# Kernel optimization log

Hardware: AMD Instinct MI355X
Metric: run time of the kernel (lower is better)

Reference implementation:

```python
import jax, jax.numpy as jnp
import numpy as np

N, IN_FEAT, OUT_FEAT = 8192, 512, 256
SLOPE = 0.1


def setup_inputs() -> dict:
    key = jax.random.key(0)
    k1, k2, k3, k4, k5 = jax.random.split(key, 5)
    doc = jax.random.normal(k1, (N, IN_FEAT), dtype=jnp.float32)
    W = jax.random.normal(k2, (IN_FEAT, OUT_FEAT), dtype=jnp.float32) * (1.0 / np.sqrt(IN_FEAT))
    W_b = jax.random.normal(k3, (OUT_FEAT,), dtype=jnp.float32) * 0.01
    a = jax.random.normal(k4, (2 * OUT_FEAT,), dtype=jnp.float32) * (1.0 / np.sqrt(2 * OUT_FEAT))
    a_b = jax.random.normal(k5, (1,), dtype=jnp.float32) * 0.01
    return {"doc": doc, "W": W, "W_b": W_b, "a": a, "a_b": a_b}


def reference(doc, W, W_b, a, a_b):
    # h = W(doc): [N, outFeat]
    h = doc @ W + W_b
    d = h.shape[-1]
    # aParams(cat(h_i, h_j)) = a1.h_i + a2.h_j + b  (avoids the O(N^2*2d) concat)
    a1, a2 = a[:d], a[d:]
    score = (h @ a1)[:, None] + (h @ a2)[None, :] + a_b[0]  # [N, N]
    score = jax.nn.leaky_relu(score, SLOPE)
    # adj=None path -> all-ones mask, the where() is a no-op
    att = jax.nn.softmax(score, axis=1)  # normalize over neighbors j
    out = jax.nn.leaky_relu(att @ h, SLOPE)  # [N, outFeat]
    return out, att
```

## Files before the change

### kernel.cpp

```cpp
#include <hip/hip_runtime.h>
#include <hip/hip_bf16.h>


typedef __attribute__((ext_vector_type(4))) float f32x4;
typedef __attribute__((ext_vector_type(8))) short short8;
typedef __attribute__((ext_vector_type(4))) unsigned short ushort4v;

#define SLOPE 0.1f
#define NROW 8192
#define DDIM 256

__device__ __forceinline__ float lrelu(float x){ return fmaxf(x, SLOPE * x); }

__device__ __forceinline__ unsigned short f2bf(float f){
  union { float f; unsigned u; } v; v.f = f;
  unsigned r = (v.u + 0x7fffu + ((v.u >> 16) & 1u)) >> 16;
  return (unsigned short)r;
}
__device__ __forceinline__ float bf2f(unsigned short u){
  union { unsigned u; float f; } v; v.u = (unsigned)u << 16; return v.f;
}
__device__ __forceinline__ unsigned cvt_pk_bf16(float lo, float hi){
  unsigned r;
  asm("v_cvt_pk_bf16_f32 %0, %1, %2" : "=v"(r) : "v"(lo), "v"(hi));
  return r;
}

__global__ __launch_bounds__(256) void k_prep(
    const float* __restrict__ W,
    unsigned short* __restrict__ Wt_hi, unsigned short* __restrict__ Wt_lo)
{
  const int tid = blockIdx.x * 256 + threadIdx.x;
  const int c = tid >> 7, kq = tid & 127;
  ushort4v hi, lo;
#pragma unroll
  for (int j = 0; j < 4; ++j) {
    const float v = W[(size_t)(kq * 4 + j) * 256 + c];
    hi[j] = f2bf(v);
    lo[j] = f2bf(v - bf2f(hi[j]));
  }
  *reinterpret_cast<ushort4v*>(Wt_hi + (size_t)c * 512 + kq * 4) = hi;
  *reinterpret_cast<ushort4v*>(Wt_lo + (size_t)c * 512 + kq * 4) = lo;
}

__global__ __launch_bounds__(512, 2) void k_h(
    const float* __restrict__ doc, const unsigned short* __restrict__ Wt_hi,
    const unsigned short* __restrict__ Wt_lo, const float* __restrict__ Wb,
    const float* __restrict__ a,
    unsigned short* __restrict__ ht, float* __restrict__ s1,
    float* __restrict__ e2, float* __restrict__ e02)
{
  __shared__ __align__(16) short8 aH[2][2][64];
  __shared__ __align__(16) short8 aL[2][2][64];
  __shared__ float sred[8][2][32];

  const int t = threadIdx.x, w = t >> 6, l = t & 63;
  const int lr = l & 15, lg = l >> 4;
  const int rb = blockIdx.x * 32;
  const int cb = w * 32;

  f32x4 acc[2][2];
#pragma unroll
  for (int rt = 0; rt < 2; ++rt)
#pragma unroll
    for (int ct = 0; ct < 2; ++ct) acc[rt][ct] = (f32x4){0.f, 0.f, 0.f, 0.f};

  const float* docp = doc + (size_t)(rb + w * 16 + lr) * 512 + lg * 8;

  f32x4 v0, v1;
  auto loadDoc = [&](int k0) { if (w < 2) {
      v0 = *reinterpret_cast<const f32x4*>(docp + k0);
      v1 = *reinterpret_cast<const f32x4*>(docp + k0 + 4);
  }};
  auto writeStage = [&](int pb) { if (w < 2) {
      union { short8 v; unsigned short u[8]; } hi, lo;
#pragma unroll
      for (int q = 0; q < 4; ++q) {
        hi.u[q] = f2bf(v0[q]);     lo.u[q] = f2bf(v0[q] - bf2f(hi.u[q]));
        hi.u[4+q] = f2bf(v1[q]);   lo.u[4+q] = f2bf(v1[q] - bf2f(hi.u[4+q]));
      }
      aH[pb][w][l] = hi.v;
      aL[pb][w][l] = lo.v;
  }};

  loadDoc(0); writeStage(0); loadDoc(32);

  for (int n = 0; n < 16; ++n) {
    const int kk = n * 32;
    const int par = n & 1;

    asm volatile("s_waitcnt lgkmcnt(0)\n\ts_barrier" ::: "memory");

    const short8 ah0 = aH[par][0][l];
    const short8 ah1 = aH[par][1][l];
    const short8 al0 = aL[par][0][l];
    const short8 al1 = aL[par][1][l];

    short8 bh[2], bl[2];
#pragma unroll
    for (int ct = 0; ct < 2; ++ct) {
      const size_t off = (size_t)(cb + ct * 16 + lr) * 512 + kk + lg * 8;
      bh[ct] = *reinterpret_cast<const short8*>(Wt_hi + off);
      bl[ct] = *reinterpret_cast<const short8*>(Wt_lo + off);
    }

    if (n + 1 < 16) writeStage(par ^ 1);
    if (n + 2 < 16) loadDoc((n + 2) * 32);

#pragma unroll
    for (int ct = 0; ct < 2; ++ct) {
      acc[0][ct] = __builtin_amdgcn_mfma_f32_16x16x32_bf16(ah0, bh[ct], acc[0][ct], 0, 0, 0);
      acc[1][ct] = __builtin_amdgcn_mfma_f32_16x16x32_bf16(ah1, bh[ct], acc[1][ct], 0, 0, 0);
      acc[0][ct] = __builtin_amdgcn_mfma_f32_16x16x32_bf16(ah0, bl[ct], acc[0][ct], 0, 0, 0);
      acc[1][ct] = __builtin_amdgcn_mfma_f32_16x16x32_bf16(ah1, bl[ct], acc[1][ct], 0, 0, 0);
      acc[0][ct] = __builtin_amdgcn_mfma_f32_16x16x32_bf16(al0, bh[ct], acc[0][ct], 0, 0, 0);
      acc[1][ct] = __builtin_amdgcn_mfma_f32_16x16x32_bf16(al1, bh[ct], acc[1][ct], 0, 0, 0);
    }
  }

  float bias[2];
#pragma unroll
  for (int ct = 0; ct < 2; ++ct) bias[ct] = Wb[cb + ct * 16 + lr];
#pragma unroll
  for (int rt = 0; rt < 2; ++rt)
#pragma unroll
    for (int ct = 0; ct < 2; ++ct) {
#pragma unroll
      for (int q = 0; q < 4; ++q) acc[rt][ct][q] += bias[ct];
      ushort4v u;
#pragma unroll
      for (int q = 0; q < 4; ++q) u[q] = f2bf(acc[rt][ct][q]);
      *reinterpret_cast<ushort4v*>(
          ht + (size_t)(cb + ct * 16 + lr) * 8192 + rb + rt * 16 + lg * 4) = u;
    }

  float a1c[2], a2c[2];
#pragma unroll
  for (int ct = 0; ct < 2; ++ct) {
    a1c[ct] = a[cb + ct * 16 + lr];
    a2c[ct] = a[256 + cb + ct * 16 + lr];
  }
  float p1[2][4], p2[2][4];
#pragma unroll
  for (int rt = 0; rt < 2; ++rt)
#pragma unroll
    for (int q = 0; q < 4; ++q) {
      float x1 = 0.f, x2 = 0.f;
#pragma unroll
      for (int ct = 0; ct < 2; ++ct) {
        x1 = fmaf(acc[rt][ct][q], a1c[ct], x1);
        x2 = fmaf(acc[rt][ct][q], a2c[ct], x2);
      }
#pragma unroll
      for (int off = 1; off < 16; off <<= 1) {
        x1 += __shfl_xor(x1, off);
        x2 += __shfl_xor(x2, off);
      }
      p1[rt][q] = x1; p2[rt][q] = x2;
    }
  __syncthreads();
  if (lr == 0) {
#pragma unroll
    for (int rt = 0; rt < 2; ++rt)
#pragma unroll
      for (int q = 0; q < 4; ++q) {
        sred[w][0][rt * 16 + lg * 4 + q] = p1[rt][q];
        sred[w][1][rt * 16 + lg * 4 + q] = p2[rt][q];
      }
  }
  __syncthreads();
  if (t < 32) {
    float v1s = 0.f, v2s = 0.f;
#pragma unroll
    for (int ww = 0; ww < 8; ++ww) { v1s += sred[ww][0][t]; v2s += sred[ww][1][t]; }
    const int r = rb + t;
    s1[r] = v1s;
    e2[r] = __expf(v2s);
    e02[r] = __expf(SLOPE * v2s);
  }
}

__global__ __launch_bounds__(256) void k_z(
    const float* __restrict__ s1, const float* __restrict__ e2g,
    const float* __restrict__ e02g, const float* __restrict__ abp,
    float* __restrict__ rowinfo)
{
  __shared__ __align__(16) float es[8192];
  __shared__ __align__(16) float fs[8192];
  const int t = threadIdx.x;
  for (int i = t * 4; i < 8192; i += 1024) {
    *reinterpret_cast<f32x4*>(&es[i]) = *reinterpret_cast<const f32x4*>(e2g + i);
    *reinterpret_cast<f32x4*>(&fs[i]) = *reinterpret_cast<const f32x4*>(e02g + i);
  }
  __syncthreads();
  const int w = t >> 6, l = t & 63;
  const float ab = abp[0];
  const int rb = blockIdx.x * 16 + w * 4;
  float T[4], E1[4], E01[4];
#pragma unroll
  for (int rr = 0; rr < 4; ++rr) {
    const float s1a = s1[rb + rr] + ab;
    E1[rr] = __expf(s1a); E01[rr] = __expf(SLOPE * s1a); T[rr] = __expf(-s1a);
  }
  float zA[4] = {0.f,0.f,0.f,0.f}, zB[4] = {0.f,0.f,0.f,0.f};
  for (int i = l * 4; i < 8192; i += 256) {
    const f32x4 e = *reinterpret_cast<const f32x4*>(&es[i]);
    const f32x4 f = *reinterpret_cast<const f32x4*>(&fs[i]);
#pragma unroll
    for (int rr = 0; rr < 4; ++rr)
#pragma unroll
      for (int q = 0; q < 4; ++q) {
        const bool c = (e[q] >= T[rr]);
        zA[rr] += c ? e[q] : 0.f;
        zB[rr] += c ? 0.f : f[q];
      }
  }
#pragma unroll
  for (int rr = 0; rr < 4; ++rr) {
    float z = E1[rr] * zA[rr] + E01[rr] * zB[rr];
#pragma unroll
    for (int off = 32; off > 0; off >>= 1) z += __shfl_down(z, off);
    if (l == 0) {
      const float iz = 1.0f / z;
      f32x4 ri = (f32x4){E1[rr] * iz, E01[rr] * iz, T[rr], iz};
      *reinterpret_cast<f32x4*>(rowinfo + (size_t)(rb + rr) * 4) = ri;
    }
  }
}

__global__ __launch_bounds__(512, 4) void k_att(
    const float* __restrict__ rowinfo, const float* __restrict__ e2g,
    const float* __restrict__ e02g, const unsigned short* __restrict__ ht,
    float* __restrict__ att, float* __restrict__ part, int CHUNK)
{
  extern __shared__ __align__(16) char smem[];
  char* plsb  = smem;
  float* e2s  = reinterpret_cast<float*>(smem + 8192);
  float* e02s = e2s + CHUNK;

  const int t = threadIdx.x, w = t >> 6, l = t & 63;
  const int lr = l & 15, lg = l >> 4;
  const int kbase = blockIdx.x * CHUNK;
  const int rb = blockIdx.y * 64;

  for (int i = t * 4; i < CHUNK; i += 2048) {
    *reinterpret_cast<f32x4*>(e2s + i)  = *reinterpret_cast<const f32x4*>(e2g + kbase + i);
    *reinterpret_cast<f32x4*>(e02s + i) = *reinterpret_cast<const f32x4*>(e02g + kbase + i);
  }

  const int r = l >> 3, jc = l & 7;
  const int rowW = rb + w * 8 + r;
  const f32x4 ri = *reinterpret_cast<const f32x4*>(rowinfo + (size_t)rowW * 4);
  const float E1z = ri[0], E01z = ri[1], T = ri[2];
  float* attW = att + (size_t)rowW * 8192 + kbase + jc * 4;
  const int fragoff = (w >> 1) * 1024 + ((jc >> 1) * 16 + (w & 1) * 8 + r) * 16 + (jc & 1) * 8;

  __syncthreads();

  auto gen = [&](int kw, int pb) {
    const f32x4 eA = *reinterpret_cast<const f32x4*>(e2s + kw + jc * 4);
    const f32x4 fA = *reinterpret_cast<const f32x4*>(e02s + kw + jc * 4);
    f32x4 pA;
#pragma unroll
    for (int q = 0; q < 4; ++q) {
      const bool cA = (eA[q] >= T);
      pA[q] = (cA ? E1z : E01z) * (cA ? eA[q] : fA[q]);
    }
    __builtin_nontemporal_store(pA, reinterpret_cast<f32x4*>(attW + kw));
    uint2 u;
    u.x = cvt_pk_bf16(pA[0], pA[1]); u.y = cvt_pk_bf16(pA[2], pA[3]);
    *reinterpret_cast<uint2*>(plsb + pb * 4096 + fragoff) = u;
  };

  const unsigned short* hbase = ht + (size_t)(w * 32 + lr) * 8192 + kbase + lg * 8;
  auto loadB = [&](short8* b, int n) {
    const int kk = n * 32;
    b[0] = *reinterpret_cast<const short8*>(hbase + kk);
    b[1] = *reinterpret_cast<const short8*>(hbase + kk + (size_t)16 * 8192);
  };

  f32x4 acc[4][2];
#pragma unroll
  for (int rt = 0; rt < 4; ++rt)
#pragma unroll
    for (int ct = 0; ct < 2; ++ct) acc[rt][ct] = (f32x4){0.f, 0.f, 0.f, 0.f};

  auto mma = [&](const short8* b, const short8& af0, const short8& af1,
                 const short8& af2, const short8& af3) {
    __builtin_amdgcn_s_setprio(1);
    acc[0][0] = __builtin_amdgcn_mfma_f32_16x16x32_bf16(af0, b[0], acc[0][0], 0, 0, 0);
    acc[1][0] = __builtin_amdgcn_mfma_f32_16x16x32_bf16(af1, b[0], acc[1][0], 0, 0, 0);
    acc[2][0] = __builtin_amdgcn_mfma_f32_16x16x32_bf16(af2, b[0], acc[2][0], 0, 0, 0);
    acc[3][0] = __builtin_amdgcn_mfma_f32_16x16x32_bf16(af3, b[0], acc[3][0], 0, 0, 0);
    acc[0][1] = __builtin_amdgcn_mfma_f32_16x16x32_bf16(af0, b[1], acc[0][1], 0, 0, 0);
    acc[1][1] = __builtin_amdgcn_mfma_f32_16x16x32_bf16(af1, b[1], acc[1][1], 0, 0, 0);
    acc[2][1] = __builtin_amdgcn_mfma_f32_16x16x32_bf16(af2, b[1], acc[2][1], 0, 0, 0);
    acc[3][1] = __builtin_amdgcn_mfma_f32_16x16x32_bf16(af3, b[1], acc[3][1], 0, 0, 0);
    __builtin_amdgcn_s_setprio(0);
  };

  short8 bAr[2], bBr[2];
  loadB(bAr, 0);
  gen(0, 0);

  const int NIT = CHUNK / 32;
  const short8* buf0 = reinterpret_cast<const short8*>(plsb);
  const short8* buf1 = reinterpret_cast<const short8*>(plsb + 4096);

  for (int n = 0; n < NIT; n += 2) {
    if (n + 1 < NIT) loadB(bBr, n + 1);
    asm volatile("s_waitcnt lgkmcnt(0)\n\ts_barrier" ::: "memory");
    {
      const short8 af0 = buf0[0 * 64 + l];
      const short8 af1 = buf0[1 * 64 + l];
      const short8 af2 = buf0[2 * 64 + l];
      const short8 af3 = buf0[3 * 64 + l];
      if (n + 1 < NIT) gen((n + 1) * 32, 1);
      mma(bAr, af0, af1, af2, af3);
    }
    if (n + 1 >= NIT) break;
    if (n + 2 < NIT) loadB(bAr, n + 2);
    asm volatile("s_waitcnt lgkmcnt(0)\n\ts_barrier" ::: "memory");
    {
      const short8 af0 = buf1[0 * 64 + l];
      const short8 af1 = buf1[1 * 64 + l];
      const short8 af2 = buf1[2 * 64 + l];
      const short8 af3 = buf1[3 * 64 + l];
      if (n + 2 < NIT) gen((n + 2) * 32, 0);
      mma(bBr, af0, af1, af2, af3);
    }
  }

  float* pb = part + (size_t)blockIdx.x * ((size_t)NROW * DDIM);
#pragma unroll
  for (int rt = 0; rt < 4; ++rt)
#pragma unroll
    for (int ct = 0; ct < 2; ++ct)
#pragma unroll
      for (int q = 0; q < 4; ++q)
        __builtin_nontemporal_store(acc[rt][ct][q],
            pb + (size_t)(rb + rt * 16 + lg * 4 + q) * 256 + w * 32 + ct * 16 + lr);
}

__global__ __launch_bounds__(256) void k_reduce(
    const float* __restrict__ part, float* __restrict__ out, int KS)
{
  const size_t idx = ((size_t)blockIdx.x * 256 + threadIdx.x) * 4;
  f32x4 s = __builtin_nontemporal_load(reinterpret_cast<const f32x4*>(part + idx));
  for (int k = 1; k < KS; ++k) {
    const f32x4 v = __builtin_nontemporal_load(
        reinterpret_cast<const f32x4*>(part + (size_t)k * NROW * DDIM + idx));
#pragma unroll
    for (int q = 0; q < 4; ++q) s[q] += v[q];
  }
#pragma unroll
  for (int q = 0; q < 4; ++q) s[q] = lrelu(s[q]);
  __builtin_nontemporal_store(s, reinterpret_cast<f32x4*>(out + idx));
}

extern "C" void kernel_launch(void* const* d_in, const int* in_sizes, int n_in,
                              void* d_out, int out_size, void* d_ws, size_t ws_size,
                              hipStream_t stream)
{
  const float* doc = (const float*)d_in[0];
  const float* W   = (const float*)d_in[1];
  const float* Wb  = (const float*)d_in[2];
  const float* a   = (const float*)d_in[3];
  const float* ab  = (const float*)d_in[4];

  float* out = (float*)d_out;
  float* att = out + (size_t)8192 * 256;

  char* ws = (char*)d_ws;
  unsigned short* ht    = (unsigned short*)ws;
  unsigned short* Wt_hi = (unsigned short*)(ws + (size_t)4 * 1024 * 1024);
  unsigned short* Wt_lo = Wt_hi + (size_t)256 * 512;
  float* s1      = (float*)(ws + (size_t)4 * 1024 * 1024 + 512 * 1024);
  float* e2      = s1 + 8192;
  float* e02     = e2 + 8192;
  float* rowinfo = e02 + 8192;
  const size_t base = (size_t)5 * 1024 * 1024;
  const size_t partBytes = (size_t)NROW * DDIM * sizeof(float);

  int KS = 1;
  for (int c = 4; c >= 1; c >>= 1)
    if (base + (size_t)c * partBytes <= ws_size) { KS = c; break; }
  float* part = (float*)(ws + base);
  const int CHUNK = NROW / KS;
  const size_t smem = 8192 + (size_t)2 * CHUNK * sizeof(float);

  hipLaunchKernelGGL(k_prep,   dim3(128),     dim3(256), 0,    stream, W, Wt_hi, Wt_lo);
  hipLaunchKernelGGL(k_h,      dim3(256),     dim3(512), 0,    stream, doc, Wt_hi, Wt_lo, Wb, a, ht, s1, e2, e02);
  hipLaunchKernelGGL(k_z,      dim3(512),     dim3(256), 0,    stream, s1, e2, e02, ab, rowinfo);
  hipLaunchKernelGGL(k_att,    dim3(KS, 128), dim3(512), smem, stream, rowinfo, e2, e02, ht, att, part, CHUNK);
  hipLaunchKernelGGL(k_reduce, dim3(2048),    dim3(256), 0,    stream, part, out, KS);
}
```

Before: 130.4 us.

## Process two k-windows per barrier phase in attention kernel, halving barriers

The attention-generation/MFMA loop now works on 64-column blocks (two 32-wide windows) per barrier phase instead of one, doubling the LDS P buffer to 16 KB and loading four B fragments per step. Each lane now computes probabilities for two rows (row and row+4) at 16 consecutive columns, which reuses the e2/e02 LDS reads and widens the contiguous att store per row. The aim is to halve the number of s_barrier/lgkmcnt waits and amortize the e2/e02 loads over more work. In exchange it uses more registers and LDS, which may lower occupancy under the 512x4 launch bounds.

```diff
diff --git a/kernel.cpp b/kernel.cpp
--- a/kernel.cpp
+++ b/kernel.cpp
@@ -235,7 +235,7 @@
 {
   extern __shared__ __align__(16) char smem[];
   char* plsb  = smem;
-  float* e2s  = reinterpret_cast<float*>(smem + 8192);
+  float* e2s  = reinterpret_cast<float*>(smem + 16384);
   float* e02s = e2s + CHUNK;
 
   const int t = threadIdx.x, w = t >> 6, l = t & 63;
@@ -248,35 +248,47 @@
     *reinterpret_cast<f32x4*>(e02s + i) = *reinterpret_cast<const f32x4*>(e02g + kbase + i);
   }
 
-  const int r = l >> 3, jc = l & 7;
-  const int rowW = rb + w * 8 + r;
-  const f32x4 ri = *reinterpret_cast<const f32x4*>(rowinfo + (size_t)rowW * 4);
-  const float E1z = ri[0], E01z = ri[1], T = ri[2];
-  float* attW = att + (size_t)rowW * 8192 + kbase + jc * 4;
-  const int fragoff = (w >> 1) * 1024 + ((jc >> 1) * 16 + (w & 1) * 8 + r) * 16 + (jc & 1) * 8;
+  const int rg = l >> 4;
+  const int k4 = (l & 15) * 4;
+  const int row0 = rb + w * 8 + rg;
+  const f32x4 ri0 = *reinterpret_cast<const f32x4*>(rowinfo + (size_t)row0 * 4);
+  const f32x4 ri1 = *reinterpret_cast<const f32x4*>(rowinfo + (size_t)(row0 + 4) * 4);
+  const float E1z0 = ri0[0], E01z0 = ri0[1], T0 = ri0[2];
+  const float E1z1 = ri1[0], E01z1 = ri1[1], T1 = ri1[2];
+  float* att0 = att + (size_t)row0 * 8192 + kbase + k4;
+  const int fragoff = ((l & 15) >> 3) * 4096 + (w >> 1) * 1024 +
+                      ((((l & 7) >> 1) * 16) + (w & 1) * 8 + rg) * 16 + (l & 1) * 8;
 
   __syncthreads();
 
-  auto gen = [&](int kw, int pb) {
-    const f32x4 eA = *reinterpret_cast<const f32x4*>(e2s + kw + jc * 4);
-    const f32x4 fA = *reinterpret_cast<const f32x4*>(e02s + kw + jc * 4);
-    f32x4 pA;
+  auto gen = [&](int bk0, int par) {
+    const f32x4 e = *reinterpret_cast<const f32x4*>(e2s + bk0 + k4);
+    const f32x4 f = *reinterpret_cast<const f32x4*>(e02s + bk0 + k4);
+    f32x4 p0, p1;
 #pragma unroll
     for (int q = 0; q < 4; ++q) {
-      const bool cA = (eA[q] >= T);
-      pA[q] = (cA ? E1z : E01z) * (cA ? eA[q] : fA[q]);
-    }
-    __builtin_nontemporal_store(pA, reinterpret_cast<f32x4*>(attW + kw));
-    uint2 u;
-    u.x = cvt_pk_bf16(pA[0], pA[1]); u.y = cvt_pk_bf16(pA[2], pA[3]);
-    *reinterpret_cast<uint2*>(plsb + pb * 4096 + fragoff) = u;
+      const bool c0 = (e[q] >= T0);
+      p0[q] = (c0 ? E1z0 : E01z0) * (c0 ? e[q] : f[q]);
+      const bool c1 = (e[q] >= T1);
+      p1[q] = (c1 ? E1z1 : E01z1) * (c1 ? e[q] : f[q]);
+    }
+    __builtin_nontemporal_store(p0, reinterpret_cast<f32x4*>(att0 + bk0));
+    __builtin_nontemporal_store(p1, reinterpret_cast<f32x4*>(att0 + bk0 + (size_t)4 * 8192));
+    uint2 u0, u1;
+    u0.x = cvt_pk_bf16(p0[0], p0[1]); u0.y = cvt_pk_bf16(p0[2], p0[3]);
+    u1.x = cvt_pk_bf16(p1[0], p1[1]); u1.y = cvt_pk_bf16(p1[2], p1[3]);
+    char* base = plsb + par * 8192 + fragoff;
+    *reinterpret_cast<uint2*>(base) = u0;
+    *reinterpret_cast<uint2*>(base + 64) = u1;
   };
 
   const unsigned short* hbase = ht + (size_t)(w * 32 + lr) * 8192 + kbase + lg * 8;
-  auto loadB = [&](short8* b, int n) {
-    const int kk = n * 32;
+  auto loadB2 = [&](short8* b, int win0) {
+    const int kk = win0 * 32;
     b[0] = *reinterpret_cast<const short8*>(hbase + kk);
     b[1] = *reinterpret_cast<const short8*>(hbase + kk + (size_t)16 * 8192);
+    b[2] = *reinterpret_cast<const short8*>(hbase + kk + 32);
+    b[3] = *reinterpret_cast<const short8*>(hbase + kk + 32 + (size_t)16 * 8192);
   };
 
   f32x4 acc[4][2];
@@ -285,50 +297,41 @@
 #pragma unroll
     for (int ct = 0; ct < 2; ++ct) acc[rt][ct] = (f32x4){0.f, 0.f, 0.f, 0.f};
 
-  auto mma = [&](const short8* b, const short8& af0, const short8& af1,
-                 const short8& af2, const short8& af3) {
+  auto mmaWin = [&](const char* wbuf, const short8& b0, const short8& b1) {
+    const short8* pbuf = reinterpret_cast<const short8*>(wbuf);
+    const short8 af0 = pbuf[0 * 64 + l];
+    const short8 af1 = pbuf[1 * 64 + l];
+    const short8 af2 = pbuf[2 * 64 + l];
+    const short8 af3 = pbuf[3 * 64 + l];
     __builtin_amdgcn_s_setprio(1);
-    acc[0][0] = __builtin_amdgcn_mfma_f32_16x16x32_bf16(af0, b[0], acc[0][0], 0, 0, 0);
-    acc[1][0] = __builtin_amdgcn_mfma_f32_16x16x32_bf16(af1, b[0], acc[1][0], 0, 0, 0);
-    acc[2][0] = __builtin_amdgcn_mfma_f32_16x16x32_bf16(af2, b[0], acc[2][0], 0, 0, 0);
-    acc[3][0] = __builtin_amdgcn_mfma_f32_16x16x32_bf16(af3, b[0], acc[3][0], 0, 0, 0);
-    acc[0][1] = __builtin_amdgcn_mfma_f32_16x16x32_bf16(af0, b[1], acc[0][1], 0, 0, 0);
-    acc[1][1] = __builtin_amdgcn_mfma_f32_16x16x32_bf16(af1, b[1], acc[1][1], 0, 0, 0);
-    acc[2][1] = __builtin_amdgcn_mfma_f32_16x16x32_bf16(af2, b[1], acc[2][1], 0, 0, 0);
-    acc[3][1] = __builtin_amdgcn_mfma_f32_16x16x32_bf16(af3, b[1], acc[3][1], 0, 0, 0);
+    acc[0][0] = __builtin_amdgcn_mfma_f32_16x16x32_bf16(af0, b0, acc[0][0], 0, 0, 0);
+    acc[1][0] = __builtin_amdgcn_mfma_f32_16x16x32_bf16(af1, b0, acc[1][0], 0, 0, 0);
+    acc[2][0] = __builtin_amdgcn_mfma_f32_16x16x32_bf16(af2, b0, acc[2][0], 0, 0, 0);
+    acc[3][0] = __builtin_amdgcn_mfma_f32_16x16x32_bf16(af3, b0, acc[3][0], 0, 0, 0);
+    acc[0][1] = __builtin_amdgcn_mfma_f32_16x16x32_bf16(af0, b1, acc[0][1], 0, 0, 0);
+    acc[1][1] = __builtin_amdgcn_mfma_f32_16x16x32_bf16(af1, b1, acc[1][1], 0, 0, 0);
+    acc[2][1] = __builtin_amdgcn_mfma_f32_16x16x32_bf16(af2, b1, acc[2][1], 0, 0, 0);
+    acc[3][1] = __builtin_amdgcn_mfma_f32_16x16x32_bf16(af3, b1, acc[3][1], 0, 0, 0);
     __builtin_amdgcn_s_setprio(0);
   };
 
-  short8 bAr[2], bBr[2];
-  loadB(bAr, 0);
+  short8 bA[4], bB[4];
+  loadB2(bA, 0);
   gen(0, 0);
 
-  const int NIT = CHUNK / 32;
-  const short8* buf0 = reinterpret_cast<const short8*>(plsb);
-  const short8* buf1 = reinterpret_cast<const short8*>(plsb + 4096);
-
-  for (int n = 0; n < NIT; n += 2) {
-    if (n + 1 < NIT) loadB(bBr, n + 1);
+  const int NB = CHUNK / 64;
+  for (int bt = 0; bt < NB; bt += 2) {
+    if (bt + 1 < NB) loadB2(bB, (bt + 1) * 2);
     asm volatile("s_waitcnt lgkmcnt(0)\n\ts_barrier" ::: "memory");
-    {
-      const short8 af0 = buf0[0 * 64 + l];
-      const short8 af1 = buf0[1 * 64 + l];
-      const short8 af2 = buf0[2 * 64 + l];
-      const short8 af3 = buf0[3 * 64 + l];
-      if (n + 1 < NIT) gen((n + 1) * 32, 1);
-      mma(bAr, af0, af1, af2, af3);
-    }
-    if (n + 1 >= NIT) break;
-    if (n + 2 < NIT) loadB(bAr, n + 2);
+    if (bt + 1 < NB) gen((bt + 1) * 64, 1);
+    mmaWin(plsb,        bA[0], bA[1]);
+    mmaWin(plsb + 4096, bA[2], bA[3]);
+    if (bt + 1 >= NB) break;
+    if (bt + 2 < NB) loadB2(bA, (bt + 2) * 2);
     asm volatile("s_waitcnt lgkmcnt(0)\n\ts_barrier" ::: "memory");
-    {
-      const short8 af0 = buf1[0 * 64 + l];
-      const short8 af1 = buf1[1 * 64 + l];
-      const short8 af2 = buf1[2 * 64 + l];
-      const short8 af3 = buf1[3 * 64 + l];
-      if (n + 2 < NIT) gen((n + 2) * 32, 0);
-      mma(bBr, af0, af1, af2, af3);
-    }
+    if (bt + 2 < NB) gen((bt + 2) * 64, 0);
+    mmaWin(plsb + 8192,  bB[0], bB[1]);
+    mmaWin(plsb + 12288, bB[2], bB[3]);
   }
 
   float* pb = part + (size_t)blockIdx.x * ((size_t)NROW * DDIM);
@@ -387,7 +390,7 @@
     if (base + (size_t)c * partBytes <= ws_size) { KS = c; break; }
   float* part = (float*)(ws + base);
   const int CHUNK = NROW / KS;
-  const size_t smem = 8192 + (size_t)2 * CHUNK * sizeof(float);
+  const size_t smem = 16384 + (size_t)2 * CHUNK * sizeof(float);
 
   hipLaunchKernelGGL(k_prep,   dim3(128),     dim3(256), 0,    stream, W, Wt_hi, Wt_lo);
   hipLaunchKernelGGL(k_h,      dim3(256),     dim3(512), 0,    stream, doc, Wt_hi, Wt_lo, Wb, a, ht, s1, e2, e02);
```

Result: slower. 149.2 us (+14.4%).

## Quad-buffer LDS probability tiles and generate two k-steps per gen call

Applied to the files above, without the earlier changes.

The attention kernel now uses four 4KB LDS buffers instead of two and produces probabilities for two consecutive 32-wide k-steps in a single gen call. That call runs only in the first half of each loop iteration, two steps ahead of consumption. This batches the exp-select, global stores and bf16 packing so more memory traffic is in flight per call, and it frees the second MMA half from generation work. The costs are higher register pressure, an uneven workload between the two loop halves, and 8KB more LDS per block, which could lower occupancy.

```diff
diff --git a/kernel.cpp b/kernel.cpp
--- a/kernel.cpp
+++ b/kernel.cpp
@@ -235,7 +235,7 @@
 {
   extern __shared__ __align__(16) char smem[];
   char* plsb  = smem;
-  float* e2s  = reinterpret_cast<float*>(smem + 8192);
+  float* e2s  = reinterpret_cast<float*>(smem + 16384);
   float* e02s = e2s + CHUNK;
 
   const int t = threadIdx.x, w = t >> 6, l = t & 63;
@@ -257,19 +257,26 @@
 
   __syncthreads();
 
-  auto gen = [&](int kw, int pb) {
+  auto gen2 = [&](int kw, int pb0, int pb1) {
     const f32x4 eA = *reinterpret_cast<const f32x4*>(e2s + kw + jc * 4);
     const f32x4 fA = *reinterpret_cast<const f32x4*>(e02s + kw + jc * 4);
-    f32x4 pA;
+    const f32x4 eB = *reinterpret_cast<const f32x4*>(e2s + kw + 32 + jc * 4);
+    const f32x4 fB = *reinterpret_cast<const f32x4*>(e02s + kw + 32 + jc * 4);
+    f32x4 pA, pB;
 #pragma unroll
     for (int q = 0; q < 4; ++q) {
       const bool cA = (eA[q] >= T);
       pA[q] = (cA ? E1z : E01z) * (cA ? eA[q] : fA[q]);
+      const bool cB = (eB[q] >= T);
+      pB[q] = (cB ? E1z : E01z) * (cB ? eB[q] : fB[q]);
     }
     __builtin_nontemporal_store(pA, reinterpret_cast<f32x4*>(attW + kw));
-    uint2 u;
-    u.x = cvt_pk_bf16(pA[0], pA[1]); u.y = cvt_pk_bf16(pA[2], pA[3]);
-    *reinterpret_cast<uint2*>(plsb + pb * 4096 + fragoff) = u;
+    __builtin_nontemporal_store(pB, reinterpret_cast<f32x4*>(attW + kw + 32));
+    uint2 uA, uB;
+    uA.x = cvt_pk_bf16(pA[0], pA[1]); uA.y = cvt_pk_bf16(pA[2], pA[3]);
+    uB.x = cvt_pk_bf16(pB[0], pB[1]); uB.y = cvt_pk_bf16(pB[2], pB[3]);
+    *reinterpret_cast<uint2*>(plsb + pb0 * 4096 + fragoff) = uA;
+    *reinterpret_cast<uint2*>(plsb + pb1 * 4096 + fragoff) = uB;
   };
 
   const unsigned short* hbase = ht + (size_t)(w * 32 + lr) * 8192 + kbase + lg * 8;
@@ -301,32 +308,29 @@
 
   short8 bAr[2], bBr[2];
   loadB(bAr, 0);
-  gen(0, 0);
+  gen2(0, 0, 1);
 
   const int NIT = CHUNK / 32;
-  const short8* buf0 = reinterpret_cast<const short8*>(plsb);
-  const short8* buf1 = reinterpret_cast<const short8*>(plsb + 4096);
-
   for (int n = 0; n < NIT; n += 2) {
-    if (n + 1 < NIT) loadB(bBr, n + 1);
+    loadB(bBr, n + 1);
     asm volatile("s_waitcnt lgkmcnt(0)\n\ts_barrier" ::: "memory");
     {
-      const short8 af0 = buf0[0 * 64 + l];
-      const short8 af1 = buf0[1 * 64 + l];
-      const short8 af2 = buf0[2 * 64 + l];
-      const short8 af3 = buf0[3 * 64 + l];
-      if (n + 1 < NIT) gen((n + 1) * 32, 1);
+      const short8* pbuf = reinterpret_cast<const short8*>(plsb + (size_t)(n & 3) * 4096);
+      const short8 af0 = pbuf[0 * 64 + l];
+      const short8 af1 = pbuf[1 * 64 + l];
+      const short8 af2 = pbuf[2 * 64 + l];
+      const short8 af3 = pbuf[3 * 64 + l];
+      if (n + 2 < NIT) gen2((n + 2) * 32, (n + 2) & 3, (n + 3) & 3);
       mma(bAr, af0, af1, af2, af3);
     }
-    if (n + 1 >= NIT) break;
     if (n + 2 < NIT) loadB(bAr, n + 2);
     asm volatile("s_waitcnt lgkmcnt(0)\n\ts_barrier" ::: "memory");
     {
-      const short8 af0 = buf1[0 * 64 + l];
-      const short8 af1 = buf1[1 * 64 + l];
-      const short8 af2 = buf1[2 * 64 + l];
-      const short8 af3 = buf1[3 * 64 + l];
-      if (n + 2 < NIT) gen((n + 2) * 32, 0);
+      const short8* pbuf = reinterpret_cast<const short8*>(plsb + (size_t)((n + 1) & 3) * 4096);
+      const short8 af0 = pbuf[0 * 64 + l];
+      const short8 af1 = pbuf[1 * 64 + l];
+      const short8 af2 = pbuf[2 * 64 + l];
+      const short8 af3 = pbuf[3 * 64 + l];
       mma(bBr, af0, af1, af2, af3);
     }
   }
@@ -387,7 +391,7 @@
     if (base + (size_t)c * partBytes <= ws_size) { KS = c; break; }
   float* part = (float*)(ws + base);
   const int CHUNK = NROW / KS;
-  const size_t smem = 8192 + (size_t)2 * CHUNK * sizeof(float);
+  const size_t smem = 16384 + (size_t)2 * CHUNK * sizeof(float);
 
   hipLaunchKernelGGL(k_prep,   dim3(128),     dim3(256), 0,    stream, W, Wt_hi, Wt_lo);
   hipLaunchKernelGGL(k_h,      dim3(256),     dim3(512), 0,    stream, doc, Wt_hi, Wt_lo, Wb, a, ht, s1, e2, e02);
```

Result: no change. 128.2 us (-1.7%).
